# Kernel tuning notes

Measured on AMD Instinct MI355X. Metric: run time of the kernel, lower is better.

Reference implementation:

```python
import jax, jax.numpy as jnp
import numpy as np

B, S_SRC, S_TGT = 16, 48, 48
H, HD, L = 512, 256, 16          # hidden, per-direction hidden, n_layers
V_IN, V_OUT = 32000, 32000


def setup_inputs() -> dict:
    key = jax.random.key(0)
    ks = jax.random.split(key, 12)
    s = 0.04  # ~1/sqrt(H), torch LSTM-style init scale
    return {
        "x": jax.random.randint(ks[0], (B, S_SRC), 0, V_IN),
        "y": jax.random.randint(ks[1], (B, S_TGT), 0, V_OUT),
        "enc_emb": jax.random.normal(ks[2], (V_IN, H), jnp.float32) * 0.2,
        "enc_W_ih": jax.random.normal(ks[3], (L, 2, 4 * HD, H), jnp.float32) * s,
        "enc_W_hh": jax.random.normal(ks[4], (L, 2, 4 * HD, HD), jnp.float32) * s,
        "enc_b": jax.random.normal(ks[5], (L, 2, 4 * HD), jnp.float32) * s,
        "dec_emb": jax.random.normal(ks[6], (V_OUT, H), jnp.float32) * 0.2,
        "dec_W_ih": jax.random.normal(ks[7], (L, 4 * H, H), jnp.float32) * s,
        "dec_W_hh": jax.random.normal(ks[8], (L, 4 * H, H), jnp.float32) * s,
        "dec_b": jax.random.normal(ks[9], (L, 4 * H), jnp.float32) * s,
        "lin_W": jax.random.normal(ks[10], (V_OUT, H), jnp.float32) * 0.2,
        "lin_b": jax.random.normal(ks[11], (V_OUT,), jnp.float32) * 0.02,
    }


def _lstm_scan(xs, h0, c0, Wih, Whh, b):
    """xs: (T, B, D). Returns (ys (T,B,Hd), hT, cT). PyTorch gate order i,f,g,o."""
    def step(carry, xt):
        h, c = carry
        g = xt @ Wih.T + h @ Whh.T + b
        i, f, gg, o = jnp.split(g, 4, axis=-1)
        c = jax.nn.sigmoid(f) * c + jax.nn.sigmoid(i) * jnp.tanh(gg)
        h = jax.nn.sigmoid(o) * jnp.tanh(c)
        return (h, c), h
    (hT, cT), ys = jax.lax.scan(step, (h0, c0), xs)
    return ys, hT, cT


def _forward(x, y, enc_emb, enc_W_ih, enc_W_hh, enc_b,
             dec_emb, dec_W_ih, dec_W_hh, dec_b, lin_W, lin_b):
    n_layers = enc_W_ih.shape[0]
    batch = x.shape[0]
    hd = enc_W_hh.shape[-1]
    dt = enc_emb.dtype

    # ---- encoder: n_layers-deep bidirectional LSTM ----
    h0 = jnp.zeros((batch, hd), dt)
    xs = enc_emb[x].transpose(1, 0, 2)  # (S_src, B, H)
    dec_h0, dec_c0 = [], []
    for l in range(n_layers):
        yf, hf, cf = _lstm_scan(xs, h0, h0, enc_W_ih[l, 0], enc_W_hh[l, 0], enc_b[l, 0])
        yb, hb, cb = _lstm_scan(xs[::-1], h0, h0, enc_W_ih[l, 1], enc_W_hh[l, 1], enc_b[l, 1])
        xs = jnp.concatenate([yf, yb[::-1]], axis=-1)  # (S, B, H)
        # torch (2L,B,Hd) -> permute/reshape -> concat(fwd,bwd) per layer
        dec_h0.append(jnp.concatenate([hf, hb], axis=-1))
        dec_c0.append(jnp.concatenate([cf, cb], axis=-1))

    # ---- decoder: teacher-forced step loop == full-sequence stacked LSTM ----
    ds = dec_emb[y].transpose(1, 0, 2)  # (S_tgt, B, H)
    for l in range(n_layers):
        ds, _, _ = _lstm_scan(ds, dec_h0[l], dec_c0[l], dec_W_ih[l], dec_W_hh[l], dec_b[l])

    logits = jnp.einsum('tbh,vh->tbv', ds, lin_W) + lin_b  # (T, B, V)
    return logits.transpose(1, 2, 0)  # (B, V_out, S_tgt) as in torch.cat(H, dim=2)


def reference(x, y, enc_emb, enc_W_ih, enc_W_hh, enc_b,
              dec_emb, dec_W_ih, dec_W_hh, dec_b, lin_W, lin_b):
    return _forward(x, y, enc_emb, enc_W_ih, enc_W_hh, enc_b,
                    dec_emb, dec_W_ih, dec_W_hh, dec_b, lin_W, lin_b)
```

## Files before the change

### kernel.cpp

```cpp
#include <hip/hip_runtime.h>
#include <stdint.h>

#define SEQ 48
#define NL  16
#define NV  32000
#define POLLMAX 4000000

typedef short bf16x8 __attribute__((ext_vector_type(8)));
typedef float f32x4  __attribute__((ext_vector_type(4)));

__device__ __forceinline__ unsigned short f2b(float f) {
    union { float f; unsigned int u; } v; v.f = f;
    unsigned int r = (v.u + 0x7FFFu + ((v.u >> 16) & 1u)) >> 16;
    return (unsigned short)r;
}
__device__ __forceinline__ float b2f(unsigned short s) {
    union { float f; unsigned int u; } v; v.u = ((unsigned int)s) << 16;
    return v.f;
}
__device__ __forceinline__ bf16x8 load_w8(const float* p) {
    const float4* q = (const float4*)p;
    float4 a = q[0], b = q[1];
    bf16x8 r;
    r[0] = (short)f2b(a.x); r[1] = (short)f2b(a.y);
    r[2] = (short)f2b(a.z); r[3] = (short)f2b(a.w);
    r[4] = (short)f2b(b.x); r[5] = (short)f2b(b.y);
    r[6] = (short)f2b(b.z); r[7] = (short)f2b(b.w);
    return r;
}
__device__ __forceinline__ bf16x8 load_b8(const unsigned short* p) {
    return *(const bf16x8*)p;
}
__device__ __forceinline__ f32x4 mfma16(bf16x8 a, bf16x8 b, f32x4 c) {
    return __builtin_amdgcn_mfma_f32_16x16x32_bf16(a, b, c, 0, 0, 0);
}
__device__ __forceinline__ float sigm(float x) { return 1.0f / (1.0f + __expf(-x)); }
__device__ __forceinline__ float tanh_(float x) { return 1.0f - 2.0f / (__expf(2.0f * x) + 1.0f); }

__global__ __launch_bounds__(256) void embed_kernel(
    const int* __restrict__ x, const int* __restrict__ y,
    const float* __restrict__ enc_emb, const float* __restrict__ dec_emb,
    unsigned short* __restrict__ xs, unsigned short* __restrict__ ds)
{
    int bid = blockIdx.x;
    int which = bid >= 768;
    int r = which ? bid - 768 : bid;
    int t = r >> 4, b = r & 15;
    int tok = which ? y[b * SEQ + t] : x[b * SEQ + t];
    const float* src = (which ? dec_emb : enc_emb) + (size_t)tok * 512;
    unsigned short* dst = (which ? ds : xs) + ((size_t)t * 16 + b) * 512;
    for (int k = threadIdx.x; k < 512; k += 256) dst[k] = f2b(src[k]);
}

__global__ __launch_bounds__(256, 2) void enc_all(
    const float* __restrict__ Wih,
    const float* __restrict__ Whh,
    const float* __restrict__ bias,
    unsigned short* __restrict__ xsA, unsigned short* __restrict__ xsB,
    unsigned short* __restrict__ dec_h0,
    float* __restrict__ dec_c0,
    int* __restrict__ flags)
{
    const int tid = threadIdx.x, bid = blockIdx.x;
    const int dir = bid >> 4, p = bid & 15;
    const int gate = tid >> 6, lane = tid & 63, q = lane >> 4, ln = lane & 15;
    __shared__ float gsm[4][16][17];
    __shared__ float cbuf[16][17];

    for (int l = 0; l < NL; ++l) {
        const unsigned short* xin = (l & 1) ? xsB : xsA;
        unsigned short* xout = (l & 1) ? xsA : xsB;
        if (l > 0) {
            if (tid < 64) {
                if (tid < 32) {
                    const int* f = flags + ((l - 1) * 32 + tid) * 16;
                    int it = 0;
                    while (__hip_atomic_load(f, __ATOMIC_RELAXED, __HIP_MEMORY_SCOPE_AGENT) < SEQ)
                        if (++it > POLLMAX) break;
                }
                __builtin_amdgcn_fence(__ATOMIC_ACQUIRE, "agent");
            }
            __syncthreads();
        }
        bf16x8 aih[16], ahh[8];
        {
            const float* wb = Wih + (((size_t)(l * 2 + dir) * 1024) + gate * 256 + p * 16 + ln) * 512;
#pragma unroll
            for (int kt = 0; kt < 16; ++kt) aih[kt] = load_w8(wb + kt * 32 + q * 8);
        }
        {
            const float* wb = Whh + (((size_t)(l * 2 + dir) * 1024) + gate * 256 + p * 16 + ln) * 256;
#pragma unroll
            for (int kt = 0; kt < 8; ++kt) ahh[kt] = load_w8(wb + kt * 32 + q * 8);
        }
        const float4 bias4 = *(const float4*)(bias + ((size_t)(l * 2 + dir) * 1024) + gate * 256 + p * 16 + q * 4);
        int* myflag = flags + (l * 32 + bid) * 16;

        for (int t = 0; t < SEQ; ++t) {
            const int t_src = dir ? (SEQ - 1 - t) : t;
            if (t > 0) {
                if (tid < 64) {
                    if (tid < 16) {
                        const int* f = flags + (l * 32 + dir * 16 + tid) * 16;
                        int it = 0;
                        while (__hip_atomic_load(f, __ATOMIC_RELAXED, __HIP_MEMORY_SCOPE_AGENT) < t)
                            if (++it > POLLMAX) break;
                    }
                    __builtin_amdgcn_fence(__ATOMIC_ACQUIRE, "agent");
                }
                __syncthreads();
            }
            f32x4 acc0 = {0.f,0.f,0.f,0.f}, acc1 = {0.f,0.f,0.f,0.f};
            const unsigned short* xrow = xin + ((size_t)t_src * 16 + ln) * 512;
#pragma unroll
            for (int kt = 0; kt < 16; kt += 2) {
                acc0 = mfma16(aih[kt],     load_b8(xrow + kt * 32 + q * 8),       acc0);
                acc1 = mfma16(aih[kt + 1], load_b8(xrow + (kt + 1) * 32 + q * 8), acc1);
            }
            if (t > 0) {
                const int prev_src = dir ? (t_src + 1) : (t_src - 1);
                const unsigned short* hrow = xout + ((size_t)prev_src * 16 + ln) * 512 + dir * 256;
#pragma unroll
                for (int kt = 0; kt < 8; kt += 2) {
                    acc0 = mfma16(ahh[kt],     load_b8(hrow + kt * 32 + q * 8),       acc0);
                    acc1 = mfma16(ahh[kt + 1], load_b8(hrow + (kt + 1) * 32 + q * 8), acc1);
                }
            }
            gsm[gate][q * 4 + 0][ln] = acc0[0] + acc1[0] + bias4.x;
            gsm[gate][q * 4 + 1][ln] = acc0[1] + acc1[1] + bias4.y;
            gsm[gate][q * 4 + 2][ln] = acc0[2] + acc1[2] + bias4.z;
            gsm[gate][q * 4 + 3][ln] = acc0[3] + acc1[3] + bias4.w;
            __syncthreads();
            if (tid < 128) {
                const int b = tid >> 3, u2 = (tid & 7) * 2;
                unsigned int hv = 0;
#pragma unroll
                for (int s = 0; s < 2; ++s) {
                    int u = u2 + s;
                    float gi = gsm[0][u][b], gf = gsm[1][u][b], gg = gsm[2][u][b], go = gsm[3][u][b];
                    float c = (t == 0) ? 0.f : cbuf[u][b];
                    float cn = sigm(gf) * c + sigm(gi) * tanh_(gg);
                    float h = sigm(go) * tanh_(cn);
                    cbuf[u][b] = cn;
                    hv |= ((unsigned int)f2b(h)) << (16 * s);
                    if (t == SEQ - 1)
                        dec_c0[((size_t)l * 16 + b) * 512 + dir * 256 + p * 16 + u] = cn;
                }
                size_t off = ((size_t)t_src * 16 + b) * 512 + dir * 256 + p * 16 + u2;
                __hip_atomic_store((unsigned int*)(xout + off), hv, __ATOMIC_RELAXED, __HIP_MEMORY_SCOPE_AGENT);
                if (t == SEQ - 1)
                    *(unsigned int*)(dec_h0 + ((size_t)l * 16 + b) * 512 + dir * 256 + p * 16 + u2) = hv;
            }
            __syncthreads();
            if (tid == 0)
                __hip_atomic_store(myflag, t + 1, __ATOMIC_RELEASE, __HIP_MEMORY_SCOPE_AGENT);
        }
    }
}

__global__ __launch_bounds__(256, 2) void dec_pipe(
    const float* __restrict__ Wih,
    const float* __restrict__ Whh,
    const float* __restrict__ bias,
    const unsigned short* __restrict__ demb,
    const unsigned short* __restrict__ h0,
    const float* __restrict__ c0,
    unsigned short* __restrict__ ds,
    int* __restrict__ flags)
{
    const int tid = threadIdx.x;
    const int l = blockIdx.x >> 5, p = blockIdx.x & 31;
    const int gate = tid >> 6, lane = tid & 63, q = lane >> 4, ln = lane & 15;
    __shared__ float gsm[4][16][17];
    __shared__ float cbuf[16][17];

    bf16x8 aih[16], ahh[16];
    const size_t row = (size_t)l * 2048 + gate * 512 + p * 16 + ln;
#pragma unroll
    for (int kt = 0; kt < 16; ++kt) aih[kt] = load_w8(Wih + row * 512 + kt * 32 + q * 8);
#pragma unroll
    for (int kt = 0; kt < 16; ++kt) ahh[kt] = load_w8(Whh + row * 512 + kt * 32 + q * 8);
    const float4 bias4 = *(const float4*)(bias + (size_t)l * 2048 + gate * 512 + p * 16 + q * 4);

    const unsigned short* xlayer = (l == 0) ? demb : (ds + (size_t)(l - 1) * SEQ * 16 * 512);
    const int* fin  = flags + (l - 1) * 32 * 16;
    const int* fown = flags + l * 32 * 16;
    int* myflag = flags + (l * 32 + p) * 16;

    for (int t = 0; t < SEQ; ++t) {
        if (tid < 64) {
            if (tid < 32) {
                if (l > 0) {
                    const int* f = fin + tid * 16;
                    int it = 0;
                    while (__hip_atomic_load(f, __ATOMIC_RELAXED, __HIP_MEMORY_SCOPE_AGENT) < t + 1)
                        if (++it > POLLMAX) break;
                }
            } else if (t > 0) {
                const int* f = fown + (tid - 32) * 16;
                int it = 0;
                while (__hip_atomic_load(f, __ATOMIC_RELAXED, __HIP_MEMORY_SCOPE_AGENT) < t)
                    if (++it > POLLMAX) break;
            }
            __builtin_amdgcn_fence(__ATOMIC_ACQUIRE, "agent");
        }
        __syncthreads();

        const unsigned short* xrow = xlayer + ((size_t)t * 16 + ln) * 512;
        const unsigned short* hrow = (t == 0) ? (h0 + ((size_t)l * 16 + ln) * 512)
                                              : (ds + (((size_t)l * SEQ + (t - 1)) * 16 + ln) * 512);
        f32x4 acc0 = {0.f,0.f,0.f,0.f}, acc1 = {0.f,0.f,0.f,0.f};
#pragma unroll
        for (int kt = 0; kt < 16; kt += 2) {
            acc0 = mfma16(aih[kt],     load_b8(xrow + kt * 32 + q * 8),       acc0);
            acc1 = mfma16(aih[kt + 1], load_b8(xrow + (kt + 1) * 32 + q * 8), acc1);
        }
#pragma unroll
        for (int kt = 0; kt < 16; kt += 2) {
            acc0 = mfma16(ahh[kt],     load_b8(hrow + kt * 32 + q * 8),       acc0);
            acc1 = mfma16(ahh[kt + 1], load_b8(hrow + (kt + 1) * 32 + q * 8), acc1);
        }
        gsm[gate][q * 4 + 0][ln] = acc0[0] + acc1[0] + bias4.x;
        gsm[gate][q * 4 + 1][ln] = acc0[1] + acc1[1] + bias4.y;
        gsm[gate][q * 4 + 2][ln] = acc0[2] + acc1[2] + bias4.z;
        gsm[gate][q * 4 + 3][ln] = acc0[3] + acc1[3] + bias4.w;
        __syncthreads();
        if (tid < 128) {
            const int b = tid >> 3, u2 = (tid & 7) * 2;
            unsigned int hv = 0;
#pragma unroll
            for (int s = 0; s < 2; ++s) {
                int u = u2 + s;
                float gi = gsm[0][u][b], gf = gsm[1][u][b], gg = gsm[2][u][b], go = gsm[3][u][b];
                float c = (t == 0) ? c0[((size_t)l * 16 + b) * 512 + p * 16 + u] : cbuf[u][b];
                float cn = sigm(gf) * c + sigm(gi) * tanh_(gg);
                float h = sigm(go) * tanh_(cn);
                cbuf[u][b] = cn;
                hv |= ((unsigned int)f2b(h)) << (16 * s);
            }
            __hip_atomic_store((unsigned int*)(ds + (((size_t)l * SEQ + t) * 16 + b) * 512 + p * 16 + u2),
                               hv, __ATOMIC_RELAXED, __HIP_MEMORY_SCOPE_AGENT);
        }
        __syncthreads();
        if (tid == 0)
            __hip_atomic_store(myflag, t + 1, __ATOMIC_RELEASE, __HIP_MEMORY_SCOPE_AGENT);
    }
}

__global__ __launch_bounds__(256) void final_gemm(
    const unsigned short* __restrict__ ds,
    const float* __restrict__ W,
    const float* __restrict__ bias,
    unsigned short* __restrict__ out)
{
    const int tid = threadIdx.x;
    const int w = tid >> 6, lane = tid & 63, q = lane >> 4, ln = lane & 15;
    const int n0 = blockIdx.x * 64;
    for (int mb = 0; mb < 12; ++mb) {
        const int m0 = mb * 64 + w * 16;
        bf16x8 afr[16];
#pragma unroll
        for (int kt = 0; kt < 16; ++kt)
            afr[kt] = load_b8(ds + ((size_t)m0 + ln) * 512 + kt * 32 + q * 8);
#pragma unroll
        for (int j = 0; j < 4; ++j) {
            f32x4 acc0 = {0.f,0.f,0.f,0.f}, acc1 = {0.f,0.f,0.f,0.f};
            const float* wb = W + ((size_t)(n0 + j * 16 + ln)) * 512;
#pragma unroll
            for (int kt = 0; kt < 16; kt += 2) {
                bf16x8 b0 = load_w8(wb + kt * 32 + q * 8);
                bf16x8 b1 = load_w8(wb + (kt + 1) * 32 + q * 8);
                acc0 = mfma16(afr[kt], b0, acc0);
                acc1 = mfma16(afr[kt + 1], b1, acc1);
            }
            int n = n0 + j * 16 + ln;
            float bv = bias[n];
#pragma unroll
            for (int r = 0; r < 4; ++r)
                out[((size_t)m0 + q * 4 + r) * NV + n] = f2b(acc0[r] + acc1[r] + bv);
        }
    }
}

__global__ __launch_bounds__(256) void transpose_out(
    const unsigned short* __restrict__ tmp, float* __restrict__ out)
{
    __shared__ unsigned short lds[256 * 50];
    const int tid = threadIdx.x;
    const int vb = blockIdx.x % 125, b = blockIdx.x / 125;
    const int v0 = vb * 256;
    for (int tt = 0; tt < SEQ; ++tt)
        lds[tid * 50 + tt] = tmp[((size_t)tt * 16 + b) * NV + v0 + tid];
    __syncthreads();
    float* ob = out + ((size_t)b * NV + v0 + tid) * SEQ;
#pragma unroll
    for (int t4 = 0; t4 < 12; ++t4) {
        float4 v;
        v.x = b2f(lds[tid * 50 + t4 * 4 + 0]);
        v.y = b2f(lds[tid * 50 + t4 * 4 + 1]);
        v.z = b2f(lds[tid * 50 + t4 * 4 + 2]);
        v.w = b2f(lds[tid * 50 + t4 * 4 + 3]);
        *(float4*)(ob + t4 * 4) = v;
    }
}

extern "C" void kernel_launch(void* const* d_in, const int* in_sizes, int n_in,
                              void* d_out, int out_size, void* d_ws, size_t ws_size,
                              hipStream_t stream)
{
    const int*   x       = (const int*)d_in[0];
    const int*   y       = (const int*)d_in[1];
    const float* enc_emb = (const float*)d_in[2];
    const float* enc_Wih = (const float*)d_in[3];
    const float* enc_Whh = (const float*)d_in[4];
    const float* enc_bb  = (const float*)d_in[5];
    const float* dec_emb = (const float*)d_in[6];
    const float* dec_Wih = (const float*)d_in[7];
    const float* dec_Whh = (const float*)d_in[8];
    const float* dec_bb  = (const float*)d_in[9];
    const float* lin_W   = (const float*)d_in[10];
    const float* lin_b   = (const float*)d_in[11];
    float* out = (float*)d_out;

    char* ws = (char*)d_ws;
    int* flags            = (int*)ws;
    unsigned short* demb  = (unsigned short*)(ws + 65536);
    unsigned short* xsA   = (unsigned short*)(ws + 65536 + 786432);
    unsigned short* xsB   = (unsigned short*)(ws + 65536 + 2 * 786432);
    unsigned short* dech0 = (unsigned short*)(ws + 65536 + 3 * 786432);
    float* decc0          = (float*)(ws + 65536 + 3 * 786432 + 262144);
    unsigned short* ds    = (unsigned short*)(ws + 65536 + 3 * 786432 + 262144 + 524288);
    unsigned short* ltmp  = (unsigned short*)(ws + 65536 + 3 * 786432 + 262144 + 524288 + (size_t)16 * 786432);

    hipMemsetAsync(flags, 0, 65536, stream);
    embed_kernel<<<1536, 256, 0, stream>>>(x, y, enc_emb, dec_emb, xsA, demb);
    enc_all<<<32, 256, 0, stream>>>(enc_Wih, enc_Whh, enc_bb, xsA, xsB, dech0, decc0, flags);
    dec_pipe<<<512, 256, 0, stream>>>(dec_Wih, dec_Whh, dec_bb, demb, dech0, decc0, ds, flags + 8192);
    final_gemm<<<500, 256, 0, stream>>>(ds + (size_t)15 * SEQ * 16 * 512, lin_W, lin_b, ltmp);
    transpose_out<<<2000, 256, 0, stream>>>(ltmp, out);
}
```

Before: 5.248 ms.

## Split encoder into input-projection producer blocks and single-block recurrent consumers

The encoder is restructured so 16 blocks precompute the input projection (W_ih·x + bias) into a float Gx buffer, and one 512-thread block per direction runs the recurrence with W_hh held in registers and LDS, and h kept in LDS. Previously 16 blocks per direction synchronized through global flags at every timestep. Now only producer/consumer flags link the two block types. The intent is to remove cross-block barrier latency from the serial recurrence and let the input GEMM of a layer overlap the recurrence of the previous one. In exchange, each timestep's recurrent matmul runs on a single CU, which adds register and LDS pressure, and the Gx buffer reuses the ds workspace.

Measured after the change: 6.840 ms. 30.3% more time.

```diff
diff --git a/kernel.cpp b/kernel.cpp
--- a/kernel.cpp
+++ b/kernel.cpp
@@ -52,109 +52,162 @@
     for (int k = threadIdx.x; k < 512; k += 256) dst[k] = f2b(src[k]);
 }
 
-__global__ __launch_bounds__(256, 2) void enc_all(
+__global__ __launch_bounds__(512, 2) void enc_v2(
     const float* __restrict__ Wih,
     const float* __restrict__ Whh,
     const float* __restrict__ bias,
     unsigned short* __restrict__ xsA, unsigned short* __restrict__ xsB,
     unsigned short* __restrict__ dec_h0,
     float* __restrict__ dec_c0,
-    int* __restrict__ flags)
+    float* __restrict__ Gx,
+    int* __restrict__ recflag,
+    int* __restrict__ gxflag)
 {
     const int tid = threadIdx.x, bid = blockIdx.x;
-    const int dir = bid >> 4, p = bid & 15;
-    const int gate = tid >> 6, lane = tid & 63, q = lane >> 4, ln = lane & 15;
-    __shared__ float gsm[4][16][17];
-    __shared__ float cbuf[16][17];
-
+    const int wv = tid >> 6, lane = tid & 63, q = lane >> 4, ln = lane & 15;
+
+    if (bid < 16) {
+        const int dir = bid >> 3, pblk = bid & 7;
+        const int gate = wv >> 1, half = wv & 1;
+        const int row0 = gate * 256 + pblk * 32 + half * 16;
+        for (int l = 0; l < NL; ++l) {
+            bf16x8 aih[16];
+            const float* wb = Wih + (((size_t)(l * 2 + dir) * 1024) + row0 + ln) * 512;
+#pragma unroll
+            for (int kt = 0; kt < 16; ++kt) aih[kt] = load_w8(wb + kt * 32 + q * 8);
+            const float4 bias4 = *(const float4*)(bias + (size_t)(l * 2 + dir) * 1024 + row0 + q * 4);
+            const unsigned short* xin = (l & 1) ? xsB : xsA;
+            float* gxl = Gx + (size_t)((l & 1) * 2 + dir) * SEQ * 16 * 1024;
+            int* myflag = gxflag + ((l * 2 + dir) * 8 + pblk) * 16;
+            const int* rfprev = recflag + (l - 1) * 2 * 16;
+            for (int s = 0; s < SEQ; ++s) {
+                const int t_src = dir ? (SEQ - 1 - s) : s;
+                if (l > 0) {
+                    if (tid < 64) {
+                        if (tid < 2) {
+                            const int need = (tid == dir) ? (s + 1) : (SEQ - s);
+                            const int* f = rfprev + tid * 16;
+                            int it = 0;
+                            while (__hip_atomic_load(f, __ATOMIC_RELAXED, __HIP_MEMORY_SCOPE_AGENT) < need)
+                                if (++it > POLLMAX) break;
+                        }
+                        __builtin_amdgcn_fence(__ATOMIC_ACQUIRE, "agent");
+                    }
+                    __syncthreads();
+                }
+                const unsigned short* xrow = xin + ((size_t)t_src * 16 + ln) * 512;
+                f32x4 acc0 = {0.f,0.f,0.f,0.f}, acc1 = {0.f,0.f,0.f,0.f};
+#pragma unroll
+                for (int kt = 0; kt < 16; kt += 2) {
+                    acc0 = mfma16(aih[kt],     load_b8(xrow + kt * 32 + q * 8),       acc0);
+                    acc1 = mfma16(aih[kt + 1], load_b8(xrow + (kt + 1) * 32 + q * 8), acc1);
+                }
+                unsigned int* gd = (unsigned int*)(gxl + ((size_t)t_src * 16 + ln) * 1024 + row0 + q * 4);
+#pragma unroll
+                for (int r = 0; r < 4; ++r) {
+                    union { float f; unsigned int u; } v;
+                    v.f = acc0[r] + acc1[r] + ((const float*)&bias4)[r];
+                    __hip_atomic_store(gd + r, v.u, __ATOMIC_RELAXED, __HIP_MEMORY_SCOPE_AGENT);
+                }
+                __syncthreads();
+                if (tid == 0)
+                    __hip_atomic_store(myflag, s + 1, __ATOMIC_RELEASE, __HIP_MEMORY_SCOPE_AGENT);
+            }
+        }
+        return;
+    }
+
+    const int dir = bid - 16;
+    __shared__ bf16x8 wlds[8][8][2][64];
+    __shared__ unsigned short h_lds[16][264];
+
+    float cr[2][4];
     for (int l = 0; l < NL; ++l) {
-        const unsigned short* xin = (l & 1) ? xsB : xsA;
+        bf16x8 wr[8][6];
+        {
+            const float* wb = Whh + (size_t)(l * 2 + dir) * 1024 * 256;
+#pragma unroll
+            for (int rt = 0; rt < 8; ++rt) {
+                const int R = (rt >> 1) * 256 + wv * 32 + (rt & 1) * 16;
+                const float* rp = wb + (size_t)(R + ln) * 256 + q * 8;
+#pragma unroll
+                for (int kt = 0; kt < 6; ++kt) wr[rt][kt] = load_w8(rp + kt * 32);
+#pragma unroll
+                for (int kt2 = 0; kt2 < 2; ++kt2)
+                    wlds[wv][rt][kt2][lane] = load_w8(rp + (6 + kt2) * 32);
+            }
+        }
+        const int* gxf = gxflag + (l * 2 + dir) * 8 * 16;
+        int* rf = recflag + (l * 2 + dir) * 16;
+        const float* gxl = Gx + (size_t)((l & 1) * 2 + dir) * SEQ * 16 * 1024;
         unsigned short* xout = (l & 1) ? xsA : xsB;
-        if (l > 0) {
-            if (tid < 64) {
-                if (tid < 32) {
-                    const int* f = flags + ((l - 1) * 32 + tid) * 16;
-                    int it = 0;
-                    while (__hip_atomic_load(f, __ATOMIC_RELAXED, __HIP_MEMORY_SCOPE_AGENT) < SEQ)
-                        if (++it > POLLMAX) break;
-                }
-                __builtin_amdgcn_fence(__ATOMIC_ACQUIRE, "agent");
-            }
-            __syncthreads();
-        }
-        bf16x8 aih[16], ahh[8];
-        {
-            const float* wb = Wih + (((size_t)(l * 2 + dir) * 1024) + gate * 256 + p * 16 + ln) * 512;
-#pragma unroll
-            for (int kt = 0; kt < 16; ++kt) aih[kt] = load_w8(wb + kt * 32 + q * 8);
-        }
-        {
-            const float* wb = Whh + (((size_t)(l * 2 + dir) * 1024) + gate * 256 + p * 16 + ln) * 256;
-#pragma unroll
-            for (int kt = 0; kt < 8; ++kt) ahh[kt] = load_w8(wb + kt * 32 + q * 8);
-        }
-        const float4 bias4 = *(const float4*)(bias + ((size_t)(l * 2 + dir) * 1024) + gate * 256 + p * 16 + q * 4);
-        int* myflag = flags + (l * 32 + bid) * 16;
+        __syncthreads();
 
         for (int t = 0; t < SEQ; ++t) {
             const int t_src = dir ? (SEQ - 1 - t) : t;
+            if (tid < 64) {
+                if (tid < 8) {
+                    const int* f = gxf + tid * 16;
+                    int it = 0;
+                    while (__hip_atomic_load(f, __ATOMIC_RELAXED, __HIP_MEMORY_SCOPE_AGENT) < t + 1)
+                        if (++it > POLLMAX) break;
+                }
+                __builtin_amdgcn_fence(__ATOMIC_ACQUIRE, "agent");
+            }
+            __syncthreads();
+            if (tid == 0 && t > 0)
+                __hip_atomic_store(rf, t, __ATOMIC_RELEASE, __HIP_MEMORY_SCOPE_AGENT);
+
+            const float* gxt = gxl + ((size_t)t_src * 16 + ln) * 1024 + wv * 32 + q * 4;
+            f32x4 acc[8];
+#pragma unroll
+            for (int rt = 0; rt < 8; ++rt) {
+                float4 g4 = *(const float4*)(gxt + (rt >> 1) * 256 + (rt & 1) * 16);
+                acc[rt][0] = g4.x; acc[rt][1] = g4.y; acc[rt][2] = g4.z; acc[rt][3] = g4.w;
+            }
             if (t > 0) {
-                if (tid < 64) {
-                    if (tid < 16) {
-                        const int* f = flags + (l * 32 + dir * 16 + tid) * 16;
-                        int it = 0;
-                        while (__hip_atomic_load(f, __ATOMIC_RELAXED, __HIP_MEMORY_SCOPE_AGENT) < t)
-                            if (++it > POLLMAX) break;
-                    }
-                    __builtin_amdgcn_fence(__ATOMIC_ACQUIRE, "agent");
-                }
-                __syncthreads();
-            }
-            f32x4 acc0 = {0.f,0.f,0.f,0.f}, acc1 = {0.f,0.f,0.f,0.f};
-            const unsigned short* xrow = xin + ((size_t)t_src * 16 + ln) * 512;
-#pragma unroll
-            for (int kt = 0; kt < 16; kt += 2) {
-                acc0 = mfma16(aih[kt],     load_b8(xrow + kt * 32 + q * 8),       acc0);
-                acc1 = mfma16(aih[kt + 1], load_b8(xrow + (kt + 1) * 32 + q * 8), acc1);
-            }
-            if (t > 0) {
-                const int prev_src = dir ? (t_src + 1) : (t_src - 1);
-                const unsigned short* hrow = xout + ((size_t)prev_src * 16 + ln) * 512 + dir * 256;
-#pragma unroll
-                for (int kt = 0; kt < 8; kt += 2) {
-                    acc0 = mfma16(ahh[kt],     load_b8(hrow + kt * 32 + q * 8),       acc0);
-                    acc1 = mfma16(ahh[kt + 1], load_b8(hrow + (kt + 1) * 32 + q * 8), acc1);
-                }
-            }
-            gsm[gate][q * 4 + 0][ln] = acc0[0] + acc1[0] + bias4.x;
-            gsm[gate][q * 4 + 1][ln] = acc0[1] + acc1[1] + bias4.y;
-            gsm[gate][q * 4 + 2][ln] = acc0[2] + acc1[2] + bias4.z;
-            gsm[gate][q * 4 + 3][ln] = acc0[3] + acc1[3] + bias4.w;
+#pragma unroll
+                for (int kt = 0; kt < 8; ++kt) {
+                    bf16x8 hf = *(const bf16x8*)&h_lds[ln][kt * 32 + q * 8];
+#pragma unroll
+                    for (int rt = 0; rt < 8; ++rt)
+                        acc[rt] = mfma16(kt < 6 ? wr[rt][kt] : wlds[wv][rt][kt - 6][lane], hf, acc[rt]);
+                }
+            }
             __syncthreads();
-            if (tid < 128) {
-                const int b = tid >> 3, u2 = (tid & 7) * 2;
-                unsigned int hv = 0;
-#pragma unroll
-                for (int s = 0; s < 2; ++s) {
-                    int u = u2 + s;
-                    float gi = gsm[0][u][b], gf = gsm[1][u][b], gg = gsm[2][u][b], go = gsm[3][u][b];
-                    float c = (t == 0) ? 0.f : cbuf[u][b];
+
+#pragma unroll
+            for (int uh = 0; uh < 2; ++uh) {
+                unsigned short hb[4];
+#pragma unroll
+                for (int r = 0; r < 4; ++r) {
+                    float gi = acc[0 + uh][r];
+                    float gf = acc[2 + uh][r];
+                    float gg = acc[4 + uh][r];
+                    float go = acc[6 + uh][r];
+                    float c  = (t == 0) ? 0.f : cr[uh][r];
                     float cn = sigm(gf) * c + sigm(gi) * tanh_(gg);
-                    float h = sigm(go) * tanh_(cn);
-                    cbuf[u][b] = cn;
-                    hv |= ((unsigned int)f2b(h)) << (16 * s);
-                    if (t == SEQ - 1)
-                        dec_c0[((size_t)l * 16 + b) * 512 + dir * 256 + p * 16 + u] = cn;
-                }
-                size_t off = ((size_t)t_src * 16 + b) * 512 + dir * 256 + p * 16 + u2;
-                __hip_atomic_store((unsigned int*)(xout + off), hv, __ATOMIC_RELAXED, __HIP_MEMORY_SCOPE_AGENT);
-                if (t == SEQ - 1)
-                    *(unsigned int*)(dec_h0 + ((size_t)l * 16 + b) * 512 + dir * 256 + p * 16 + u2) = hv;
-            }
-            __syncthreads();
-            if (tid == 0)
-                __hip_atomic_store(myflag, t + 1, __ATOMIC_RELEASE, __HIP_MEMORY_SCOPE_AGENT);
-        }
+                    cr[uh][r] = cn;
+                    hb[r] = f2b(sigm(go) * tanh_(cn));
+                }
+                const int u = wv * 32 + uh * 16 + q * 4;
+                uint2 hv;
+                hv.x = (unsigned)hb[0] | ((unsigned)hb[1] << 16);
+                hv.y = (unsigned)hb[2] | ((unsigned)hb[3] << 16);
+                *(uint2*)&h_lds[ln][u] = hv;
+                unsigned int* xo = (unsigned int*)(xout + ((size_t)t_src * 16 + ln) * 512 + dir * 256 + u);
+                __hip_atomic_store(xo,     hv.x, __ATOMIC_RELAXED, __HIP_MEMORY_SCOPE_AGENT);
+                __hip_atomic_store(xo + 1, hv.y, __ATOMIC_RELAXED, __HIP_MEMORY_SCOPE_AGENT);
+                if (t == SEQ - 1) {
+                    *(uint2*)(dec_h0 + ((size_t)l * 16 + ln) * 512 + dir * 256 + u) = hv;
+                    float4 cv; cv.x = cr[uh][0]; cv.y = cr[uh][1]; cv.z = cr[uh][2]; cv.w = cr[uh][3];
+                    *(float4*)(dec_c0 + ((size_t)l * 16 + ln) * 512 + dir * 256 + u) = cv;
+                }
+            }
+        }
+        __syncthreads();
+        if (tid == 0)
+            __hip_atomic_store(rf, SEQ, __ATOMIC_RELEASE, __HIP_MEMORY_SCOPE_AGENT);
     }
 }
 
@@ -332,9 +385,11 @@
     unsigned short* ds    = (unsigned short*)(ws + 65536 + 3 * 786432 + 262144 + 524288);
     unsigned short* ltmp  = (unsigned short*)(ws + 65536 + 3 * 786432 + 262144 + 524288 + (size_t)16 * 786432);
 
+    float* Gx = (float*)ds;
     hipMemsetAsync(flags, 0, 65536, stream);
     embed_kernel<<<1536, 256, 0, stream>>>(x, y, enc_emb, dec_emb, xsA, demb);
-    enc_all<<<32, 256, 0, stream>>>(enc_Wih, enc_Whh, enc_bb, xsA, xsB, dech0, decc0, flags);
+    enc_v2<<<18, 512, 0, stream>>>(enc_Wih, enc_Whh, enc_bb, xsA, xsB, dech0, decc0,
+                                   Gx, flags, flags + 512);
     dec_pipe<<<512, 256, 0, stream>>>(dec_Wih, dec_Whh, dec_bb, demb, dech0, decc0, ds, flags + 8192);
     final_gemm<<<500, 256, 0, stream>>>(ds + (size_t)15 * SEQ * 16 * 512, lin_W, lin_b, ltmp);
     transpose_out<<<2000, 256, 0, stream>>>(ltmp, out);
```
